# Performance work log

Hardware: AMD Instinct MI355X
Metric: run time of the kernel (lower is better)

## Reference

```python
import jax, jax.numpy as jnp
import numpy as np

B, S, HID = 1, 4096, 2048
NH, D = 16, 128
RATIO, TOPK, WIN = 4, 8, 128
ROPE_DIM = D // 2  # partial RoPE on first half of head_dim
EPS = 1e-6
NEG = -1e30


def rmsnorm(x, w):
    return x * jax.lax.rsqrt(jnp.mean(x * x, axis=-1, keepdims=True) + EPS) * w


def apply_rope(x, pos):
    # x: [..., L, D_head]; pos: [L] integer positions
    half = ROPE_DIM // 2
    inv = 1.0 / (10000.0 ** (jnp.arange(half, dtype=x.dtype) * (2.0 / ROPE_DIM)))
    ang = pos.astype(x.dtype)[:, None] * inv[None, :]  # [L, half]
    cos, sin = jnp.cos(ang), jnp.sin(ang)
    x1, x2, rest = x[..., :half], x[..., half:ROPE_DIM], x[..., ROPE_DIM:]
    return jnp.concatenate([x1 * cos - x2 * sin, x1 * sin + x2 * cos, rest], axis=-1)


def setup_inputs() -> dict:
    key = jax.random.key(0)
    ks = jax.random.split(key, 16)
    n = jax.random.normal
    s = 0.02
    return {
        "hidden_states": n(ks[0], (B, S, HID), jnp.float32),
        "Wq": n(ks[1], (HID, NH * D)) * s, "bq": jnp.zeros((NH * D,)),
        "Wcmp": n(ks[2], (HID, 1)) * s, "bcmp": jnp.zeros((1,)),
        "Wk": n(ks[3], (HID, D)) * s, "bk": jnp.zeros((D,)),
        "Wv": n(ks[4], (HID, D)) * s, "bv": jnp.zeros((D,)),
        "Wlk": n(ks[5], (HID, NH * D)) * s, "blk": jnp.zeros((NH * D,)),
        "Wlv": n(ks[6], (HID, NH * D)) * s, "blv": jnp.zeros((NH * D,)),
        "qn_w": jnp.ones((D,)), "kn_w": jnp.ones((D,)),
        "Wo": n(ks[7], (NH * D, HID)) * s, "bo": jnp.zeros((HID,)),
    }


def reference(hidden_states, Wq, bq, Wcmp, bcmp, Wk, bk, Wv, bv, Wlk, blk, Wlv, blv, qn_w, kn_w, Wo, bo):
    Bq, Sq, _ = hidden_states.shape
    C = Sq // RATIO
    scale = 1.0 / jnp.sqrt(jnp.float32(D))
    pos = jnp.arange(Sq)

    q = (hidden_states @ Wq + bq).reshape(Bq, Sq, NH, D).transpose(0, 2, 1, 3)  # [B,H,S,D]
    q = apply_rope(rmsnorm(q, qn_w), pos)

    # learned KV compression: softmax-weighted pooling within each block of size RATIO
    w_log = (hidden_states @ Wcmp + bcmp).reshape(Bq, C, RATIO)
    w_cmp = jax.nn.softmax(w_log, axis=-1)
    entries = jnp.einsum('bcr,bcrh->bch', w_cmp, hidden_states.reshape(Bq, C, RATIO, HID))
    block_ends = jnp.arange(1, C + 1) * RATIO - 1  # [C] last position of each block

    ck = apply_rope(rmsnorm(entries @ Wk + bk, kn_w), block_ends)  # [B,C,D] shared kv head
    cv = entries @ Wv + bv  # [B,C,D]

    # top-k block-sparse attention over compressed entries (causal on block_ends)
    sc = jnp.einsum('bhsd,bcd->bhsc', q, ck) * scale  # [B,H,S,C]
    causal = block_ends[None, None, None, :] <= pos[None, None, :, None]
    sc = jnp.where(causal, sc, NEG)
    tv, ti = jax.lax.top_k(sc, TOPK)  # [B,H,S,K]
    sel = (tv > NEG / 2).astype(sc.dtype)
    m = jnp.max(tv, axis=-1, keepdims=True)
    e = jnp.exp(tv - m) * sel
    pw = e / jnp.maximum(e.sum(axis=-1, keepdims=True), 1e-9)
    v_g = cv[jnp.arange(Bq)[:, None, None, None], ti]  # [B,H,S,K,D] irregular gather
    ctx_sparse = jnp.einsum('bhsk,bhskd->bhsd', pw, v_g)

    lk = apply_rope(rmsnorm((hidden_states @ Wlk + blk).reshape(Bq, Sq, NH, D).transpose(0, 2, 1, 3), kn_w), pos)
    lv = (hidden_states @ Wlv + blv).reshape(Bq, Sq, NH, D).transpose(0, 2, 1, 3)
    nc = Sq // WIN
    qc = q.reshape(Bq, NH, nc, WIN, D)

    def windowize(x):
        prev = jnp.pad(x, ((0, 0), (0, 0), (WIN, 0), (0, 0)))[:, :, :-WIN].reshape(Bq, NH, nc, WIN, D)
        cur = x.reshape(Bq, NH, nc, WIN, D)
        return jnp.concatenate([prev, cur], axis=3)  # [B,H,nc,2W,D]

    kw, vw = windowize(lk), windowize(lv)
    i = jnp.arange(WIN)[:, None]
    j = jnp.arange(2 * WIN)[None, :]
    rel = i + WIN - j  # qpos - kpos within the chunk pair
    band = (rel >= 0) & (rel <= WIN)
    kpos_ok = (jnp.arange(nc)[:, None, None] * WIN - WIN + j[None]) >= 0  # zero-pad chunk invalid
    mask = band[None] & kpos_ok  # [nc,W,2W]
    sl = jnp.einsum('bhcqd,bhckd->bhcqk', qc, kw) * scale
    sl = jnp.where(mask[None, None], sl, NEG)
    pl = jax.nn.softmax(sl, axis=-1)
    ctx_local = jnp.einsum('bhcqk,bhckd->bhcqd', pl, vw).reshape(Bq, NH, Sq, D)

    merged = (ctx_sparse + ctx_local) * 0.5  # mean over the two branches
    out = merged.transpose(0, 2, 1, 3).reshape(Bq, Sq, NH * D) @ Wo + bo
    return out
```

## Files before the change

### kernel.cpp

```cpp
#include <hip/hip_runtime.h>
#include <hip/hip_bf16.h>
#include <hip/hip_fp16.h>
#include <stdint.h>

typedef __hip_bfloat16 bf16;
using bf16x8 = __attribute__((ext_vector_type(8))) short;
using half8  = __attribute__((ext_vector_type(8))) _Float16;
using f32x4  = __attribute__((ext_vector_type(4))) float;

#define S_LEN   4096
#define HID_    2048
#define NH_     16
#define D_      128
#define C_      1024
#define SCALE_  0.08838834764831845f
#define DESC_   (1.0 / 1048576.0)

__device__ __forceinline__ void storeC(float* p, float v) { *p = v; }
__device__ __forceinline__ void storeC(bf16* p, float v)  { *p = __float2bfloat16(v); }
__device__ __forceinline__ void split2(float x, _Float16& h, _Float16& l) {
  h = (_Float16)x; l = (_Float16)(x - (float)h);
}
__device__ __forceinline__ short bf2s(bf16 b) { short s; __builtin_memcpy(&s, &b, 2); return s; }

#define GLDS(src, dst) __builtin_amdgcn_global_load_lds( \
    (const __attribute__((address_space(1))) void*)(src), \
    (__attribute__((address_space(3))) void*)(dst), 16, 0, 0)


__device__ __forceinline__ void cvt_bias_body(int bxx, const float* __restrict__ src, bf16* __restrict__ dst,
                                              const float* bq, const float* blk, const float* blv,
                                              const float* bk, const float* bv, const float* bo,
                                              float* bQ, float* bLKLV, float* bKV, float* bO) {
  int i = (bxx * 256 + threadIdx.x) * 4;
  float4 v = *(const float4*)(src + i);
  bf16 o[4] = {__float2bfloat16(v.x), __float2bfloat16(v.y),
               __float2bfloat16(v.z), __float2bfloat16(v.w)};
  *(uint2*)(dst + i) = *(uint2*)o;
  int ib = bxx * 256 + threadIdx.x;
  if (ib < 8448) {
    if (ib < 2048)      bQ[ib] = bq[ib];
    else if (ib < 6144) { int j = ib - 2048; bLKLV[j] = (j < 2048) ? blk[j] : blv[j - 2048]; }
    else if (ib < 6400) { int j = ib - 6144; bKV[j] = (j < 128) ? bk[j] : bv[j - 128]; }
    else                bO[ib - 6400] = bo[ib - 6400];
  }
}

__device__ __forceinline__ void transpose3_body(int bxx, int byy, int bzz, char* smem,
                                                const float* __restrict__ Wlk, const float* __restrict__ Wlv,
                                                const float* __restrict__ Wo,
                                                bf16* __restrict__ bt_lklv, bf16* __restrict__ WoT) {
  float (*tile)[65] = (float(*)[65])smem;
  const float* src = (bzz == 0) ? Wlk : (bzz == 1) ? Wlv : Wo;
  bf16* dst = (bzz == 0) ? bt_lklv
            : (bzz == 1) ? (bt_lklv + (size_t)2048 * HID_) : WoT;
  const int c0 = bxx * 64, r0 = byy * 64;
  const int t = threadIdx.x, cc = t & 63, rb = t >> 6;
#pragma unroll
  for (int i = 0; i < 16; ++i) {
    int r = rb + i * 4;
    tile[r][cc] = src[(size_t)(r0 + r) * HID_ + c0 + cc];
  }
  __syncthreads();
#pragma unroll
  for (int i = 0; i < 16; ++i) {
    int r = rb + i * 4;
    dst[(size_t)(c0 + r) * HID_ + r0 + cc] = __float2bfloat16(tile[cc][r]);
  }
}

__device__ __forceinline__ void trans_kv_body(int bxx, int byy, int bzz, char* smem,
                                              const float* __restrict__ Wk, const float* __restrict__ Wv,
                                              float* __restrict__ WkvTs) {
  float (*tile)[65] = (float(*)[65])smem;
  const float* src = bzz ? Wv : Wk;
  float* dst = WkvTs + (bzz ? (size_t)128 * HID_ : 0);
  const int c0 = bxx * 64, r0 = byy * 64;
  const int t = threadIdx.x, cc = t & 63, rb = t >> 6;
#pragma unroll
  for (int i = 0; i < 16; ++i) {
    int r = rb + i * 4;
    tile[r][cc] = src[(size_t)(r0 + r) * 128 + c0 + cc];
  }
  __syncthreads();
#pragma unroll
  for (int i = 0; i < 16; ++i) {
    int r = rb + i * 4;
    dst[(size_t)(c0 + r) * HID_ + r0 + cc] = tile[cc][r] * 1024.0f;
  }
}

__device__ __forceinline__ void wlog_body(int bxx, const float* __restrict__ hidden,
                                          const float* __restrict__ wcmp, const float* __restrict__ bcmp,
                                          float* __restrict__ wlog) {
  int s = bxx * 4 + (threadIdx.x >> 6);
  int lane = threadIdx.x & 63;
  const float* hp = hidden + (size_t)s * HID_;
  double acc = 0.0;
  for (int i = lane; i < HID_; i += 64)
    acc += (double)hp[i] * (double)wcmp[i];
#pragma unroll
  for (int m = 32; m; m >>= 1) acc += __shfl_xor(acc, m, 64);
  if (lane == 0) wlog[s] = (float)(acc + (double)bcmp[0]);
}

__device__ __forceinline__ void split_q_body(int bxx, const float* __restrict__ src,
                                             _Float16* __restrict__ oh, _Float16* __restrict__ ol) {
  int i = (bxx * 256 + threadIdx.x) * 4;
  float4 v = *(const float4*)(src + i);
  float xs[4] = {v.x, v.y, v.z, v.w};
  _Float16 hh[4], ll[4];
#pragma unroll
  for (int e = 0; e < 4; ++e) split2(xs[e] * 1024.0f, hh[e], ll[e]);
  *(uint2*)(oh + i) = *(uint2*)hh;
  *(uint2*)(ol + i) = *(uint2*)ll;
}

__device__ __forceinline__ void trans_split_wq_body(int bxx, int byy, char* smem,
                                                    const float* __restrict__ src,
                                                    _Float16* __restrict__ oh, _Float16* __restrict__ ol) {
  float (*tile)[65] = (float(*)[65])smem;
  const int c0 = bxx * 64, r0 = byy * 64;
  const int t = threadIdx.x, cc = t & 63, rb = t >> 6;
#pragma unroll
  for (int i = 0; i < 16; ++i) {
    int r = rb + i * 4;
    tile[r][cc] = src[(size_t)(r0 + r) * HID_ + c0 + cc];
  }
  __syncthreads();
#pragma unroll
  for (int i = 0; i < 16; ++i) {
    int r = rb + i * 4;
    float x = tile[cc][r] * 1024.0f;
    _Float16 h, l; split2(x, h, l);
    size_t off = (size_t)(c0 + r) * HID_ + r0 + cc;
    oh[off] = h; ol[off] = l;
  }
}

__device__ __forceinline__ void entries_body(int bxx, const float* __restrict__ hidden,
                                             const float* __restrict__ wsm, float* __restrict__ entriesF) {
  int idx = bxx * 256 + threadIdx.x;
  int c = idx >> 11, hcol = idx & 2047;
  double e = 0.0;
#pragma unroll
  for (int r = 0; r < 4; ++r)
    e += (double)wsm[4 * c + r] * (double)hidden[(size_t)(4 * c + r) * HID_ + hcol];
  entriesF[idx] = (float)e;
}

template <typename OutT>
__device__ __forceinline__ void gemm_bt_body(int bxp, int byp, bf16* As, bf16* Bs,
                                             const bf16* __restrict__ A, const bf16* __restrict__ BT,
                                             const float* __restrict__ bias, OutT* __restrict__ Cmat,
                                             int M, int N, int K, int lda) {
  const int t = threadIdx.x;
  const int wave = t >> 6, lane = t & 63;
  const int wr = wave >> 1, wc = wave & 1;
  const int quad = lane >> 4, l15 = lane & 15;
  const int bx = bxp * 128, by = byp * 128;
  const int srow = t >> 2, scol = (t & 3) * 8;
  f32x4 acc[4][4] = {};
  const bf16* a0 = A + (size_t)(by + srow) * lda + scol;
  const bf16* a1 = A + (size_t)(by + 64 + srow) * lda + scol;
  const bf16* b0 = BT + (size_t)(bx + srow) * K + scol;
  const bf16* b1 = BT + (size_t)(bx + 64 + srow) * K + scol;
  for (int k0 = 0; k0 < K; k0 += 32) {
    GLDS(a0 + k0, As + t * 8);
    GLDS(a1 + k0, As + 2048 + t * 8);
    GLDS(b0 + k0, Bs + t * 8);
    GLDS(b1 + k0, Bs + 2048 + t * 8);
    __syncthreads();
    bf16x8 aF[4], bF[4];
#pragma unroll
    for (int i = 0; i < 4; ++i)
      aF[i] = *(const bf16x8*)(As + (wr * 64 + i * 16 + l15) * 32 + quad * 8);
#pragma unroll
    for (int j = 0; j < 4; ++j)
      bF[j] = *(const bf16x8*)(Bs + (wc * 64 + j * 16 + l15) * 32 + quad * 8);
#pragma unroll
    for (int i = 0; i < 4; ++i)
#pragma unroll
      for (int j = 0; j < 4; ++j)
        acc[i][j] = __builtin_amdgcn_mfma_f32_16x16x32_bf16(aF[i], bF[j], acc[i][j], 0, 0, 0);
    __syncthreads();
  }
#pragma unroll
  for (int i = 0; i < 4; ++i)
#pragma unroll
    for (int j = 0; j < 4; ++j)
#pragma unroll
      for (int r = 0; r < 4; ++r) {
        int row = by + wr * 64 + i * 16 + quad * 4 + r;
        int col = bx + wc * 64 + j * 16 + l15;
        storeC(&Cmat[(size_t)row * N + col], acc[i][j][r] + bias[col]);
      }
}

__device__ __forceinline__ void gemm_hl4_body(int bxp, int byp, _Float16* Ahs, _Float16* Als,
                                              _Float16* Bhs, _Float16* Bls,
                                              const _Float16* __restrict__ Ah, const _Float16* __restrict__ Al,
                                              const _Float16* __restrict__ Bh, const _Float16* __restrict__ Bl,
                                              const float* __restrict__ bias, float* __restrict__ Cmat,
                                              int M, int N, int K, int lda) {
  const int t = threadIdx.x;
  const int wave = t >> 6, lane = t & 63;
  const int wr = wave >> 1, wc = wave & 1;
  const int quad = lane >> 4, l15 = lane & 15;
  const int bx = bxp * 128, by = byp * 128;
  const int srow = t >> 2, scol = (t & 3) * 8;
  double acc[4][4][4] = {};
  const _Float16* a0h = Ah + (size_t)(by + srow) * lda + scol;
  const _Float16* a1h = Ah + (size_t)(by + 64 + srow) * lda + scol;
  const _Float16* a0l = Al + (size_t)(by + srow) * lda + scol;
  const _Float16* a1l = Al + (size_t)(by + 64 + srow) * lda + scol;
  const _Float16* b0h = Bh + (size_t)(bx + srow) * K + scol;
  const _Float16* b1h = Bh + (size_t)(bx + 64 + srow) * K + scol;
  const _Float16* b0l = Bl + (size_t)(bx + srow) * K + scol;
  const _Float16* b1l = Bl + (size_t)(bx + 64 + srow) * K + scol;
  for (int k0 = 0; k0 < K; k0 += 32) {
    GLDS(a0h + k0, Ahs + t * 8);
    GLDS(a1h + k0, Ahs + 2048 + t * 8);
    GLDS(a0l + k0, Als + t * 8);
    GLDS(a1l + k0, Als + 2048 + t * 8);
    GLDS(b0h + k0, Bhs + t * 8);
    GLDS(b1h + k0, Bhs + 2048 + t * 8);
    GLDS(b0l + k0, Bls + t * 8);
    GLDS(b1l + k0, Bls + 2048 + t * 8);
    __syncthreads();
    half8 aFh[4], aFl[4], bFh[4], bFl[4];
#pragma unroll
    for (int i = 0; i < 4; ++i) {
      int ro = (wr * 64 + i * 16 + l15) * 32 + quad * 8;
      aFh[i] = *(const half8*)(Ahs + ro);
      aFl[i] = *(const half8*)(Als + ro);
    }
#pragma unroll
    for (int j = 0; j < 4; ++j) {
      int ro = (wc * 64 + j * 16 + l15) * 32 + quad * 8;
      bFh[j] = *(const half8*)(Bhs + ro);
      bFl[j] = *(const half8*)(Bls + ro);
    }
#pragma unroll
    for (int i = 0; i < 4; ++i)
#pragma unroll
      for (int j = 0; j < 4; ++j) {
        f32x4 tt = {0.f, 0.f, 0.f, 0.f};
        tt = __builtin_amdgcn_mfma_f32_16x16x32_f16(aFl[i], bFl[j], tt, 0, 0, 0);
        tt = __builtin_amdgcn_mfma_f32_16x16x32_f16(aFl[i], bFh[j], tt, 0, 0, 0);
        tt = __builtin_amdgcn_mfma_f32_16x16x32_f16(aFh[i], bFl[j], tt, 0, 0, 0);
        tt = __builtin_amdgcn_mfma_f32_16x16x32_f16(aFh[i], bFh[j], tt, 0, 0, 0);
#pragma unroll
        for (int r = 0; r < 4; ++r) acc[i][j][r] += (double)tt[r];
      }
    __syncthreads();
  }
#pragma unroll
  for (int i = 0; i < 4; ++i)
#pragma unroll
    for (int j = 0; j < 4; ++j)
#pragma unroll
      for (int r = 0; r < 4; ++r) {
        int row = by + wr * 64 + i * 16 + quad * 4 + r;
        int col = bx + wc * 64 + j * 16 + l15;
        Cmat[(size_t)row * N + col] = (float)(acc[i][j][r] * DESC_ + (double)bias[col]);
      }
}

__device__ __forceinline__ void gemm_prec4_body(int bxp, int byp, _Float16* Ah, _Float16* Al,
                                                _Float16* Bh, _Float16* Bl,
                                                const float* __restrict__ A, const float* __restrict__ BT,
                                                const float* __restrict__ bias, float* __restrict__ Cmat,
                                                int M, int N, int K, int lda) {
  const int t = threadIdx.x;
  const int wave = t >> 6, lane = t & 63;
  const int wr = wave >> 1, wc = wave & 1;
  const int quad = lane >> 4, l15 = lane & 15;
  const int bx = bxp * 128, by = byp * 128;
  double acc[4][4][4] = {};
  for (int k0 = 0; k0 < K; k0 += 32) {
#pragma unroll
    for (int it = 0; it < 4; ++it) {
      int sl = t + it * 256;
      int isB = sl >> 9, s2 = sl & 511, r = s2 >> 2, g = s2 & 3;
      const float* src = isB ? (BT + (size_t)(bx + r) * K + k0 + g * 8)
                             : (A  + (size_t)(by + r) * lda + k0 + g * 8);
      float4 u = ((const float4*)src)[0];
      float4 v = ((const float4*)src)[1];
      float xs[8] = {u.x, u.y, u.z, u.w, v.x, v.y, v.z, v.w};
      half8 hh, ll;
#pragma unroll
      for (int e = 0; e < 8; ++e) {
        float x = isB ? xs[e] : xs[e] * 1024.0f;
        _Float16 h, l; split2(x, h, l);
        hh[e] = h; ll[e] = l;
      }
      _Float16* dh = (isB ? Bh : Ah) + r * 32 + g * 8;
      _Float16* dl = (isB ? Bl : Al) + r * 32 + g * 8;
      *(half8*)dh = hh;
      *(half8*)dl = ll;
    }
    __syncthreads();
    half8 aFh[4], aFl[4], bFh[4], bFl[4];
#pragma unroll
    for (int i = 0; i < 4; ++i) {
      int ro = (wr * 64 + i * 16 + l15) * 32 + quad * 8;
      aFh[i] = *(const half8*)(Ah + ro);
      aFl[i] = *(const half8*)(Al + ro);
    }
#pragma unroll
    for (int j = 0; j < 4; ++j) {
      int ro = (wc * 64 + j * 16 + l15) * 32 + quad * 8;
      bFh[j] = *(const half8*)(Bh + ro);
      bFl[j] = *(const half8*)(Bl + ro);
    }
#pragma unroll
    for (int i = 0; i < 4; ++i)
#pragma unroll
      for (int j = 0; j < 4; ++j) {
        f32x4 tt = {0.f, 0.f, 0.f, 0.f};
        tt = __builtin_amdgcn_mfma_f32_16x16x32_f16(aFl[i], bFl[j], tt, 0, 0, 0);
        tt = __builtin_amdgcn_mfma_f32_16x16x32_f16(aFl[i], bFh[j], tt, 0, 0, 0);
        tt = __builtin_amdgcn_mfma_f32_16x16x32_f16(aFh[i], bFl[j], tt, 0, 0, 0);
        tt = __builtin_amdgcn_mfma_f32_16x16x32_f16(aFh[i], bFh[j], tt, 0, 0, 0);
#pragma unroll
        for (int r = 0; r < 4; ++r) acc[i][j][r] += (double)tt[r];
      }
    __syncthreads();
  }
#pragma unroll
  for (int i = 0; i < 4; ++i)
#pragma unroll
    for (int j = 0; j < 4; ++j)
#pragma unroll
      for (int r = 0; r < 4; ++r) {
        int row = by + wr * 64 + i * 16 + quad * 4 + r;
        int col = bx + wc * 64 + j * 16 + l15;
        Cmat[(size_t)row * N + col] = (float)(acc[i][j][r] * DESC_ + (double)bias[col]);
      }
}

__device__ __forceinline__ void normrope_q_body(int s, double* csd, double* snd,
                                                float* __restrict__ base, const float* __restrict__ w,
                                                _Float16* __restrict__ qh, _Float16* __restrict__ ql) {
  const int t = threadIdx.x, wv = t >> 6, lane = t & 63;
  if (t < 32) {
    float invf = 1.0f / (float)pow(10000.0, (double)t * (1.0 / 32.0));
    float angf = (float)s * invf;
    double ang = (double)angf;
    csd[t] = cos(ang);
    snd[t] = sin(ang);
  }
  __syncthreads();
  const int fi = lane & 31;
  float* ps = base + (size_t)s * HID_;
  for (int h = wv; h < 16; h += 4) {
    float* p = ps + h * 128;
    double x0 = (double)p[lane];
    double x1 = (double)p[lane + 64];
    double ss = x0 * x0 + x1 * x1;
#pragma unroll
    for (int m = 32; m; m >>= 1) ss += __shfl_xor(ss, m, 64);
    double rstd = 1.0 / sqrt(ss * (1.0 / 128.0) + 1e-6);
    double n0 = x0 * rstd * (double)w[lane];
    double n1 = x1 * rstd * (double)w[lane + 64];
    double other = __shfl_xor(n0, 32, 64);
    double cs = csd[fi], sn = snd[fi];
    double r0 = (lane < 32) ? (n0 * cs - other * sn) : (other * sn + n0 * cs);
    float f0 = (float)r0, f1 = (float)n1;
    p[lane] = f0;
    p[lane + 64] = f1;
    _Float16 h0, l0, h1, l1;
    split2(f0 * 1024.0f, h0, l0);
    split2(f1 * 1024.0f, h1, l1);
    size_t off = (size_t)s * HID_ + h * 128;
    qh[off + lane] = h0;       ql[off + lane] = l0;
    qh[off + 64 + lane] = h1;  ql[off + 64 + lane] = l1;
  }
}

__device__ __forceinline__ void normrope_ck_body(int bxx, float* __restrict__ base, const float* __restrict__ w,
                                                 _Float16* __restrict__ ckh, _Float16* __restrict__ ckl) {
  int row = bxx * 4 + (threadIdx.x >> 6);
  int lane = threadIdx.x & 63;
  float* p = base + (size_t)row * 256;
  double x0 = (double)p[lane];
  double x1 = (double)p[lane + 64];
  double ss = x0 * x0 + x1 * x1;
#pragma unroll
  for (int m = 32; m; m >>= 1) ss += __shfl_xor(ss, m, 64);
  double rstd = 1.0 / sqrt(ss * (1.0 / 128.0) + 1e-6);
  double n0 = x0 * rstd * (double)w[lane];
  double n1 = x1 * rstd * (double)w[lane + 64];
  double other = __shfl_xor(n0, 32, 64);
  int fi = lane & 31;
  float invf = 1.0f / (float)pow(10000.0, (double)fi * (1.0 / 32.0));
  float angf = (float)(row * 4 + 3) * invf;
  double ang = (double)angf;
  double cs = cos(ang), sn = sin(ang);
  double r0 = (lane < 32) ? (n0 * cs - other * sn) : (other * sn + n0 * cs);
  float f0 = (float)r0, f1 = (float)n1;
  p[lane] = f0;
  p[lane + 64] = f1;
  _Float16 h0, l0, h1, l1;
  split2(f0 * 1024.0f, h0, l0);
  split2(f1 * 1024.0f, h1, l1);
  ckh[row * 128 + lane] = h0;       ckl[row * 128 + lane] = l0;
  ckh[row * 128 + 64 + lane] = h1;  ckl[row * 128 + 64 + lane] = l1;
}

__device__ __forceinline__ void normrope_bfl_body(int s, float* csf, float* snf,
                                                  bf16* __restrict__ base, const float* __restrict__ w) {
  const int t = threadIdx.x, wv = t >> 6, lane = t & 63;
  if (t < 32) {
    float invf = 1.0f / (float)pow(10000.0, (double)t * (1.0 / 32.0));
    float ang = (float)s * invf;
    csf[t] = cosf(ang);
    snf[t] = sinf(ang);
  }
  __syncthreads();
  const int fi = lane & 31;
  bf16* ps = base + (size_t)s * 4096;
  for (int h = wv; h < 16; h += 4) {
    bf16* p = ps + h * 128;
    float x0 = __bfloat162float(p[lane]);
    float x1 = __bfloat162float(p[lane + 64]);
    float ss = x0 * x0 + x1 * x1;
#pragma unroll
    for (int m = 32; m; m >>= 1) ss += __shfl_xor(ss, m, 64);
    float rstd = rsqrtf(ss * 0.0078125f + 1e-6f);
    float n0 = x0 * rstd * w[lane];
    float n1 = x1 * rstd * w[lane + 64];
    float other = __shfl_xor(n0, 32, 64);
    float cs = csf[fi], sn = snf[fi];
    float r0 = (lane < 32) ? (n0 * cs - other * sn) : (other * sn + n0 * cs);
    p[lane] = __float2bfloat16(r0);
    p[lane + 64] = __float2bfloat16(n1);
  }
}


__global__ __launch_bounds__(256) void prep_fused(const float* hidden, bf16* hbf,
                                                  const float* Wlk, const float* Wlv, const float* Wo,
                                                  bf16* bt_lklv, bf16* WoT,
                                                  const float* Wk, const float* Wv, float* WkvTs,
                                                  const float* wcmp, const float* bcmp, float* wlog,
                                                  const float* bq, const float* blk, const float* blv,
                                                  const float* bk, const float* bv, const float* bo,
                                                  float* bQ, float* bLKLV, float* bKV, float* bO) {
  __shared__ __align__(16) char smem[16640];
  int b = blockIdx.x;
  if (b < 3072) {
    int z = b >> 10, rem = b & 1023;
    transpose3_body(rem & 31, rem >> 5, z, smem, Wlk, Wlv, Wo, bt_lklv, WoT);
  } else if (b < 3200) {
    int tt = b - 3072;
    trans_kv_body(tt & 1, (tt & 63) >> 1, tt >> 6, smem, Wk, Wv, WkvTs);
  } else if (b < 11392) {
    cvt_bias_body(b - 3200, hidden, hbf, bq, blk, blv, bk, bv, bo, bQ, bLKLV, bKV, bO);
  } else {
    wlog_body(b - 11392, hidden, wcmp, bcmp, wlog);
  }
}

__global__ void wsm_k(const float* __restrict__ wlog, float* __restrict__ wsm) {
  int c = blockIdx.x * 256 + threadIdx.x;
  if (c >= C_) return;
  double v[4], m = -1e300;
#pragma unroll
  for (int r = 0; r < 4; ++r) { v[r] = (double)wlog[4 * c + r]; if (v[r] > m) m = v[r]; }
  double sum = 0.0;
#pragma unroll
  for (int r = 0; r < 4; ++r) { v[r] = exp(v[r] - m); sum += v[r]; }
#pragma unroll
  for (int r = 0; r < 4; ++r) wsm[4 * c + r] = (float)(v[r] / sum);
}

__global__ __launch_bounds__(256) void lklv_entries_fused(const bf16* hbf, const bf16* bt_lklv,
                                                          const float* bLKLV, bf16* lklv,
                                                          const float* hidden, const float* wsm,
                                                          float* entriesF) {
  __shared__ __align__(16) bf16 AsBs[2][4096];
  int b = blockIdx.x;
  if (b < 1024) {
    gemm_bt_body<bf16>(b & 31, b >> 5, AsBs[0], AsBs[1], hbf, bt_lklv, bLKLV, lklv,
                       S_LEN, 4096, HID_, HID_);
  } else {
    entries_body(b - 1024, hidden, wsm, entriesF);
  }
}

__global__ __launch_bounds__(256) void splitq_fused(const float* hidden, _Float16* hidh, _Float16* hidl,
                                                    const float* Wq, _Float16* wqh, _Float16* wql) {
  __shared__ __align__(16) char smem[16640];
  int b = blockIdx.x;
  if (b < 1024) {
    trans_split_wq_body(b & 31, b >> 5, smem, Wq, wqh, wql);
  } else {
    split_q_body(b - 1024, hidden, hidh, hidl);
  }
}

__global__ __launch_bounds__(256) void qgemm_fused(const _Float16* hidh, const _Float16* hidl,
                                                   const _Float16* wqh, const _Float16* wql,
                                                   const float* bQ, float* qf,
                                                   const float* entriesF, const float* WkvTs,
                                                   const float* bKV, float* ckvF) {
  __shared__ __align__(16) _Float16 SH4[4][4096];
  int b = blockIdx.x;
  if (b < 512) {
    gemm_hl4_body(b & 15, b >> 4, SH4[0], SH4[1], SH4[2], SH4[3],
                  hidh, hidl, wqh, wql, bQ, qf, S_LEN, HID_, HID_, HID_);
  } else {
    int tt = b - 512;
    gemm_prec4_body(tt & 1, tt >> 1, SH4[0], SH4[1], SH4[2], SH4[3],
                    entriesF, WkvTs, bKV, ckvF, C_, 256, HID_, HID_);
  }
}

__global__ __launch_bounds__(256) void normrope_fused(float* qf, const float* qn_w,
                                                      _Float16* qh, _Float16* ql,
                                                      float* ckvF, const float* kn_w,
                                                      _Float16* ckh, _Float16* ckl,
                                                      bf16* lklv) {
  __shared__ double csd[32], snd[32];
  __shared__ float csf[32], snf[32];
  int b = blockIdx.x;
  if (b < 256) {
    normrope_ck_body(b, ckvF, kn_w, ckh, ckl);
  } else if (b < 4352) {
    normrope_q_body(b - 256, csd, snd, qf, qn_w, qh, ql);
  } else {
    normrope_bfl_body(b - 4352, csf, snf, lklv, kn_w);
  }
}

__global__ __launch_bounds__(256) void trans_v_k(const bf16* __restrict__ lklv, bf16* __restrict__ VT) {
  __shared__ ushort tile[64][65];
  const int s0 = blockIdx.x * 64, c0 = blockIdx.y * 64;
  const int t = threadIdx.x, cc = t & 63, rb = t >> 6;
  const ushort* src = (const ushort*)lklv;
#pragma unroll
  for (int i = 0; i < 16; ++i) {
    int r = rb + i * 4;
    tile[r][cc] = src[(size_t)(s0 + r) * 4096 + 2048 + c0 + cc];
  }
  __syncthreads();
  ushort* dst = (ushort*)VT;
#pragma unroll
  for (int i = 0; i < 16; ++i) {
    int r = rb + i * 4;
    dst[(size_t)(c0 + r) * 4096 + s0 + cc] = tile[cc][r];
  }
}

template <typename OutT>
__global__ __launch_bounds__(256) void gemm_bt(const bf16* __restrict__ A, const bf16* __restrict__ BT,
                                               const float* __restrict__ bias, OutT* __restrict__ Cmat,
                                               int M, int N, int K, int lda) {
  __shared__ __align__(16) bf16 AsBs[2][4096];
  gemm_bt_body<OutT>(blockIdx.x, blockIdx.y, AsBs[0], AsBs[1], A, BT, bias, Cmat, M, N, K, lda);
}

__global__ __launch_bounds__(1024, 8) void sparse_v9(const _Float16* __restrict__ qh, const _Float16* __restrict__ ql,
                                                     const _Float16* __restrict__ ckh, const _Float16* __restrict__ ckl,
                                                     const float* __restrict__ ckvF, bf16* __restrict__ sp) {
  __shared__ float sc[16 * 1024];
  const int by = blockIdx.y;
  const int s0 = blockIdx.x * 8;
  const int t = threadIdx.x, w = t >> 6, lane = t & 63;
  const int quad = lane >> 4, l15 = lane & 15;
  const int nvmax  = (s0 >> 2) + 2;
  const int ntiles = (nvmax + 15) >> 4;
  const double esc = (double)SCALE_ * DESC_;

  if (w < ntiles) {
    const int sA = s0 + (l15 & 7);
    const int hA = 2 * by + (l15 >> 3);
    half8 aFh[4], aFl[4];
    {
      const _Float16* qbh = qh + (size_t)sA * HID_ + hA * 128 + quad * 8;
      const _Float16* qbl = ql + (size_t)sA * HID_ + hA * 128 + quad * 8;
#pragma unroll
      for (int kk = 0; kk < 4; ++kk) {
        aFh[kk] = *(const half8*)(qbh + kk * 32);
        aFl[kk] = *(const half8*)(qbl + kk * 32);
      }
    }
    for (int ct = w; ct < ntiles; ct += 16) {
      const int c0 = ct * 16;
      const _Float16* kbh = ckh + (size_t)(c0 + l15) * 128 + quad * 8;
      const _Float16* kbl = ckl + (size_t)(c0 + l15) * 128 + quad * 8;
      double a64[4] = {0.0, 0.0, 0.0, 0.0};
#pragma unroll
      for (int kk = 0; kk < 4; ++kk) {
        half8 bh = *(const half8*)(kbh + kk * 32);
        half8 bl = *(const half8*)(kbl + kk * 32);
        f32x4 tt = {0.f, 0.f, 0.f, 0.f};
        tt = __builtin_amdgcn_mfma_f32_16x16x32_f16(aFl[kk], bl, tt, 0, 0, 0);
        tt = __builtin_amdgcn_mfma_f32_16x16x32_f16(aFl[kk], bh, tt, 0, 0, 0);
        tt = __builtin_amdgcn_mfma_f32_16x16x32_f16(aFh[kk], bl, tt, 0, 0, 0);
        tt = __builtin_amdgcn_mfma_f32_16x16x32_f16(aFh[kk], bh, tt, 0, 0, 0);
#pragma unroll
        for (int r = 0; r < 4; ++r) a64[r] += (double)tt[r];
      }
#pragma unroll
      for (int r = 0; r < 4; ++r)
        sc[(quad * 4 + r) * 1024 + c0 + l15] = (float)(a64[r] * esc);
    }
  }
  __syncthreads();
  if (w >= 4) return;

  const int q = w * 4 + quad;
  const int p2 = q >> 3, wq = q & 7;
  const int s = s0 + wq;
  const int nv = (s >= 3) ? (((s - 3) >> 2) + 1) : 0;
  const float* srow = sc + q * 1024;
  const int jmaxB = (nvmax + 63) >> 6;

  float tv0 = -1e38f, tv1 = -1e38f, tv2 = -1e38f, tv3 = -1e38f;
  int   ti0 = 0x40000000, ti1 = 0x40000000, ti2 = 0x40000000, ti3 = 0x40000000;
  for (int j = 0; j < jmaxB; ++j) {
    int cb = j * 64 + l15 * 4;
    float4 vv = *(const float4*)(srow + cb);
    float xs[4] = {vv.x, vv.y, vv.z, vv.w};
#pragma unroll
    for (int e = 0; e < 4; ++e) {
      int c = cb + e;
      float v = (c < nv) ? xs[e] : -1e38f;
      if (v > tv3) {
        if (v > tv0)      { tv3=tv2;ti3=ti2; tv2=tv1;ti2=ti1; tv1=tv0;ti1=ti0; tv0=v;ti0=c; }
        else if (v > tv1) { tv3=tv2;ti3=ti2; tv2=tv1;ti2=ti1; tv1=v;ti1=c; }
        else if (v > tv2) { tv3=tv2;ti3=ti2; tv2=v;ti2=c; }
        else              { tv3=v;ti3=c; }
      }
    }
  }

  unsigned long long deadm = 0ull;
  int ncons = 0;
  float bvs[8]; int bis[8];
#pragma unroll
  for (int it = 0; it < 8; ++it) {
    float bv = tv0; int bi = ti0;
#pragma unroll
    for (int mm = 1; mm <= 8; mm <<= 1) {
      float ov = __shfl_xor(bv, mm, 64);
      int   oi = __shfl_xor(bi, mm, 64);
      if (ov > bv || (ov == bv && oi < bi)) { bv = ov; bi = oi; }
    }
    bvs[it] = bv; bis[it] = bi;
    if (bv > -1e29f && (((bi >> 2) & 15) == l15)) {
      deadm |= 1ull << (((bi >> 6) << 2) | (bi & 3));
      tv0=tv1;ti0=ti1; tv1=tv2;ti1=ti2; tv2=tv3;ti2=ti3;
      tv3=-1e38f; ti3=0x40000000;
      if (++ncons == 4) {
        ncons = 0;
        tv0=tv1=tv2=tv3=-1e38f;
        ti0=ti1=ti2=ti3=0x40000000;
        for (int j = 0; j < jmaxB; ++j) {
          int cb = j * 64 + l15 * 4;
          float4 vv = *(const float4*)(srow + cb);
          float xs[4] = {vv.x, vv.y, vv.z, vv.w};
#pragma unroll
          for (int e = 0; e < 4; ++e) {
            int c = cb + e;
            int li = ((c >> 6) << 2) | (c & 3);
            float v = (c < nv && !((deadm >> li) & 1ull)) ? xs[e] : -1e38f;
            if (v > tv3) {
              if (v > tv0)      { tv3=tv2;ti3=ti2; tv2=tv1;ti2=ti1; tv1=tv0;ti1=ti0; tv0=v;ti0=c; }
              else if (v > tv1) { tv3=tv2;ti3=ti2; tv2=tv1;ti2=ti1; tv1=v;ti1=c; }
              else if (v > tv2) { tv3=tv2;ti3=ti2; tv2=v;ti2=c; }
              else              { tv3=v;ti3=c; }
            }
          }
        }
      }
    }
  }

  const float m0 = bvs[0];
  float a0=0.f,a1=0.f,a2=0.f,a3=0.f,a4=0.f,a5=0.f,a6=0.f,a7=0.f;
  float esum = 0.f;
#pragma unroll
  for (int it = 0; it < 8; ++it) {
    if (bvs[it] > -1e29f) {
      float wgt = expf(bvs[it] - m0);
      esum += wgt;
      const float* cvp = ckvF + (size_t)bis[it] * 256 + 128 + l15 * 8;
      float4 u = *(const float4*)cvp;
      float4 v = *(const float4*)(cvp + 4);
      a0 += wgt*u.x; a1 += wgt*u.y; a2 += wgt*u.z; a3 += wgt*u.w;
      a4 += wgt*v.x; a5 += wgt*v.y; a6 += wgt*v.z; a7 += wgt*v.w;
    }
  }
  float inv = 1.0f / fmaxf(esum, 1e-9f);
  bf16* op = sp + (size_t)s * 2048 + (2 * by + p2) * 128 + l15 * 8;
  bf16 ob[8] = {__float2bfloat16(a0*inv), __float2bfloat16(a1*inv),
                __float2bfloat16(a2*inv), __float2bfloat16(a3*inv),
                __float2bfloat16(a4*inv), __float2bfloat16(a5*inv),
                __float2bfloat16(a6*inv), __float2bfloat16(a7*inv)};
  *(uint4*)op = *(uint4*)ob;
}

__global__ __launch_bounds__(128) void local_mfma(const float* __restrict__ qf,
                                                  const bf16* __restrict__ lklv,
                                                  const bf16* __restrict__ VT,
                                                  const bf16* __restrict__ sp,
                                                  bf16* __restrict__ merged) {
  constexpr int PADP = 168;
  __shared__ bf16 PhS[2][16 * PADP];
  __shared__ bf16 PlS[2][16 * PADP];
  const int h = blockIdx.y;
  const int t = threadIdx.x, w = t >> 6, lane = t & 63;
  const int quad = lane >> 4, l15 = lane & 15;
  const int sw = blockIdx.x * 32 + w * 16;
  const int kbase = sw - 128;
  const int ridx = quad * 4;

  bf16x8 qH[4], qL[4];
  {
    const float* qp = qf + (size_t)(sw + l15) * HID_ + h * 128 + quad * 8;
#pragma unroll
    for (int kk = 0; kk < 4; ++kk) {
      float4 u = *(const float4*)(qp + kk * 32);
      float4 v = *(const float4*)(qp + kk * 32 + 4);
      float xs[8] = {u.x, u.y, u.z, u.w, v.x, v.y, v.z, v.w};
      bf16x8 hh, ll;
#pragma unroll
      for (int e = 0; e < 8; ++e) {
        bf16 bh = __float2bfloat16(xs[e]);
        float fh = __bfloat162float(bh);
        bf16 bl = __float2bfloat16(xs[e] - fh);
        hh[e] = bf2s(bh); ll[e] = bf2s(bl);
      }
      qH[kk] = hh; qL[kk] = ll;
    }
  }

  float sc[9][4];
#pragma unroll
  for (int ct = 0; ct < 9; ++ct) {
    int key0 = kbase + ct * 16 + l15;
    const bf16* kp = lklv + (size_t)(key0 < 0 ? 0 : key0) * 4096 + h * 128 + quad * 8;
    f32x4 acc = {0.f, 0.f, 0.f, 0.f};
#pragma unroll
    for (int kk = 0; kk < 4; ++kk) {
      bf16x8 kb = *(const bf16x8*)(kp + kk * 32);
      acc = __builtin_amdgcn_mfma_f32_16x16x32_bf16(qL[kk], kb, acc, 0, 0, 0);
      acc = __builtin_amdgcn_mfma_f32_16x16x32_bf16(qH[kk], kb, acc, 0, 0, 0);
    }
#pragma unroll
    for (int r = 0; r < 4; ++r) sc[ct][r] = acc[r] * SCALE_;
  }

  float mrow[4] = {-1e30f, -1e30f, -1e30f, -1e30f};
#pragma unroll
  for (int ct = 0; ct < 9; ++ct) {
    int cidx = ct * 16 + l15;
#pragma unroll
    for (int r = 0; r < 4; ++r) {
      bool valid = (cidx >= ridx + r) && (cidx <= ridx + r + 128) && (kbase + cidx >= 0);
      float v = valid ? sc[ct][r] : -1e30f;
      sc[ct][r] = v;
      mrow[r] = fmaxf(mrow[r], v);
    }
  }
#pragma unroll
  for (int mm = 1; mm <= 8; mm <<= 1)
#pragma unroll
    for (int r = 0; r < 4; ++r) mrow[r] = fmaxf(mrow[r], __shfl_xor(mrow[r], mm, 64));

  bf16* phb = &PhS[w][0];
  bf16* plb = &PlS[w][0];
  for (int z = lane; z < 256; z += 64) {
    int zr = z >> 4, zc = z & 15;
    phb[zr * PADP + 144 + zc] = __float2bfloat16(0.f);
    plb[zr * PADP + 144 + zc] = __float2bfloat16(0.f);
  }
  float lsum[4] = {0.f, 0.f, 0.f, 0.f};
#pragma unroll
  for (int ct = 0; ct < 9; ++ct) {
    int cidx = ct * 16 + l15;
#pragma unroll
    for (int r = 0; r < 4; ++r) {
      float e = (sc[ct][r] > -1e29f) ? expf(sc[ct][r] - mrow[r]) : 0.f;
      lsum[r] += e;
      bf16 bh = __float2bfloat16(e);
      float fh = __bfloat162float(bh);
      bf16 bl = __float2bfloat16(e - fh);
      phb[(ridx + r) * PADP + cidx] = bh;
      plb[(ridx + r) * PADP + cidx] = bl;
    }
  }
#pragma unroll
  for (int mm = 1; mm <= 8; mm <<= 1)
#pragma unroll
    for (int r = 0; r < 4; ++r) lsum[r] += __shfl_xor(lsum[r], mm, 64);
  float inv[4];
#pragma unroll
  for (int r = 0; r < 4; ++r) inv[r] = 1.0f / lsum[r];

  bf16x8 pH[5], pL[5];
#pragma unroll
  for (int kk = 0; kk < 5; ++kk) {
    pH[kk] = *(const bf16x8*)(phb + l15 * PADP + kk * 32 + quad * 8);
    pL[kk] = *(const bf16x8*)(plb + l15 * PADP + kk * 32 + quad * 8);
  }

#pragma unroll
  for (int dt = 0; dt < 8; ++dt) {
    const bf16* vrow = VT + (size_t)(h * 128 + dt * 16 + l15) * 4096;
    f32x4 acc = {0.f, 0.f, 0.f, 0.f};
#pragma unroll
    for (int kk = 0; kk < 5; ++kk) {
      int ko = kbase + kk * 32 + quad * 8;
      ko = ko < 0 ? 0 : (ko > 4088 ? 4088 : ko);
      bf16x8 vb = *(const bf16x8*)(vrow + ko);
      acc = __builtin_amdgcn_mfma_f32_16x16x32_bf16(pL[kk], vb, acc, 0, 0, 0);
      acc = __builtin_amdgcn_mfma_f32_16x16x32_bf16(pH[kk], vb, acc, 0, 0, 0);
    }
#pragma unroll
    for (int r = 0; r < 4; ++r) {
      int srow = sw + ridx + r;
      size_t off = (size_t)srow * 2048 + h * 128 + dt * 16 + l15;
      float spv = __bfloat162float(sp[off]);
      merged[off] = __float2bfloat16((acc[r] * inv[r] + spv) * 0.5f);
    }
  }
}

extern "C" void kernel_launch(void* const* d_in, const int* in_sizes, int n_in,
                              void* d_out, int out_size, void* d_ws, size_t ws_size,
                              hipStream_t stream) {
  (void)in_sizes; (void)n_in; (void)out_size; (void)ws_size;
  const float* hidden = (const float*)d_in[0];
  const float* Wq   = (const float*)d_in[1];
  const float* bq   = (const float*)d_in[2];
  const float* Wcmp = (const float*)d_in[3];
  const float* bcmp = (const float*)d_in[4];
  const float* Wk   = (const float*)d_in[5];
  const float* bk   = (const float*)d_in[6];
  const float* Wv   = (const float*)d_in[7];
  const float* bv   = (const float*)d_in[8];
  const float* Wlk  = (const float*)d_in[9];
  const float* blk  = (const float*)d_in[10];
  const float* Wlv  = (const float*)d_in[11];
  const float* blv  = (const float*)d_in[12];
  const float* qn_w = (const float*)d_in[13];
  const float* kn_w = (const float*)d_in[14];
  const float* Wo   = (const float*)d_in[15];
  const float* bo   = (const float*)d_in[16];
  float* out = (float*)d_out;

  char* ws = (char*)d_ws;
  float*    qf       = (float*)   (ws);
  bf16*     lklv     = (bf16*)    (ws + 33554432);
  _Float16* qh       = (_Float16*)(ws + 67108864);
  bf16*     VT       = (bf16*)    (ws + 67108864);
  bf16*     hbf      = (bf16*)    (ws + 83886080);
  _Float16* hidh     = (_Float16*)(ws + 83886080);
  bf16*     merged   = (bf16*)    (ws + 83886080);
  bf16*     bt_lklv  = (bf16*)    (ws + 100663296);
  _Float16* hidl     = (_Float16*)(ws + 100663296);
  bf16*     sp       = (bf16*)    (ws + 100663296);
  float*    WkvTs    = (float*)   (ws + 117440512);
  bf16*     WoT      = (bf16*)    (ws + 119537664);
  float*    entriesF = (float*)   (ws + 127926272);
  float*    ckvF     = (float*)   (ws + 136314880);
  _Float16* ckh      = (_Float16*)(ws + 137363456);
  _Float16* ckl      = (_Float16*)(ws + 137625600);
  float*    wlog     = (float*)   (ws + 137887744);
  float*    wsm      = (float*)   (ws + 137904128);
  float*    bQ       = (float*)   (ws + 137920512);
  float*    bLKLV    = (float*)   (ws + 137928704);
  float*    bKV      = (float*)   (ws + 137945088);
  float*    bO       = (float*)   (ws + 137946112);
  _Float16* wqh      = (_Float16*)(ws + 137954304);
  _Float16* wql      = (_Float16*)(ws + 146342912);
  _Float16* ql       = (_Float16*)(ws + 137954304);

  prep_fused<<<dim3(12416), dim3(256), 0, stream>>>(hidden, hbf, Wlk, Wlv, Wo, bt_lklv, WoT,
                                                    Wk, Wv, WkvTs, Wcmp, bcmp, wlog,
                                                    bq, blk, blv, bk, bv, bo, bQ, bLKLV, bKV, bO);
  wsm_k<<<dim3(4), dim3(256), 0, stream>>>(wlog, wsm);
  lklv_entries_fused<<<dim3(9216), dim3(256), 0, stream>>>(hbf, bt_lklv, bLKLV, lklv,
                                                           hidden, wsm, entriesF);
  splitq_fused<<<dim3(9216), dim3(256), 0, stream>>>(hidden, hidh, hidl, Wq, wqh, wql);
  qgemm_fused<<<dim3(528), dim3(256), 0, stream>>>(hidh, hidl, wqh, wql, bQ, qf,
                                                   entriesF, WkvTs, bKV, ckvF);
  normrope_fused<<<dim3(8448), dim3(256), 0, stream>>>(qf, qn_w, qh, ql, ckvF, kn_w, ckh, ckl, lklv);
  sparse_v9<<<dim3(512, 8), dim3(1024), 0, stream>>>(qh, ql, ckh, ckl, ckvF, sp);
  trans_v_k<<<dim3(64, 32), dim3(256), 0, stream>>>(lklv, VT);
  local_mfma<<<dim3(128, 16), dim3(128), 0, stream>>>(qf, lklv, VT, sp, merged);
  gemm_bt<float><<<dim3(16, 32), dim3(256), 0, stream>>>(merged, WoT, bO, out, S_LEN, HID_, HID_, HID_);
}
```

Baseline: 997.7 us.

## Halve Q-GEMM tile width, swizzle LDS fragments, schedule slow blocks first

The split-half fp16 Q projection GEMM now uses 128x64 tiles instead of 128x128, which doubles the block count so more blocks are in flight on the GPU, and halves the double-precision accumulator registers per thread. Global-to-LDS loads use an XOR swizzle on the 8-element column groups, and fragment reads undo it, to reduce LDS bank conflicts. The long-K ck/cv precision GEMM blocks are moved to the front of the grid so they start early. The cost is less operand reuse per tile, since each A tile is now loaded twice as often.

After: 887.7 us. -11.0%, faster.

```diff
diff --git a/kernel.cpp b/kernel.cpp
--- a/kernel.cpp
+++ b/kernel.cpp
@@ -197,54 +197,55 @@
       }
 }
 
-__device__ __forceinline__ void gemm_hl4_body(int bxp, int byp, _Float16* Ahs, _Float16* Als,
-                                              _Float16* Bhs, _Float16* Bls,
-                                              const _Float16* __restrict__ Ah, const _Float16* __restrict__ Al,
-                                              const _Float16* __restrict__ Bh, const _Float16* __restrict__ Bl,
-                                              const float* __restrict__ bias, float* __restrict__ Cmat,
-                                              int M, int N, int K, int lda) {
+__device__ __forceinline__ void gemm_hl4b_body(int bxp, int byp, _Float16* Ahs, _Float16* Als,
+                                               _Float16* Bhs, _Float16* Bls,
+                                               const _Float16* __restrict__ Ah, const _Float16* __restrict__ Al,
+                                               const _Float16* __restrict__ Bh, const _Float16* __restrict__ Bl,
+                                               const float* __restrict__ bias, float* __restrict__ Cmat,
+                                               int N, int K, int lda) {
   const int t = threadIdx.x;
   const int wave = t >> 6, lane = t & 63;
   const int wr = wave >> 1, wc = wave & 1;
   const int quad = lane >> 4, l15 = lane & 15;
-  const int bx = bxp * 128, by = byp * 128;
-  const int srow = t >> 2, scol = (t & 3) * 8;
-  double acc[4][4][4] = {};
-  const _Float16* a0h = Ah + (size_t)(by + srow) * lda + scol;
-  const _Float16* a1h = Ah + (size_t)(by + 64 + srow) * lda + scol;
-  const _Float16* a0l = Al + (size_t)(by + srow) * lda + scol;
-  const _Float16* a1l = Al + (size_t)(by + 64 + srow) * lda + scol;
-  const _Float16* b0h = Bh + (size_t)(bx + srow) * K + scol;
-  const _Float16* b1h = Bh + (size_t)(bx + 64 + srow) * K + scol;
-  const _Float16* b0l = Bl + (size_t)(bx + srow) * K + scol;
-  const _Float16* b1l = Bl + (size_t)(bx + 64 + srow) * K + scol;
+  const int bx = bxp * 64, by = byp * 128;
+  const int rA0 = t >> 2;
+  const int rA1 = rA0 + 64;
+  const int g   = t & 3;
+  const int gsA0 = g ^ ((rA0 >> 1) & 3);
+  const int gsA1 = g ^ ((rA1 >> 1) & 3);
+  const int swz  = (l15 >> 1) & 3;
+  double acc[4][2][4] = {};
+  const _Float16* a0h = Ah + (size_t)(by + rA0) * lda + gsA0 * 8;
+  const _Float16* a1h = Ah + (size_t)(by + rA1) * lda + gsA1 * 8;
+  const _Float16* a0l = Al + (size_t)(by + rA0) * lda + gsA0 * 8;
+  const _Float16* a1l = Al + (size_t)(by + rA1) * lda + gsA1 * 8;
+  const _Float16* b0h = Bh + (size_t)(bx + rA0) * K + gsA0 * 8;
+  const _Float16* b0l = Bl + (size_t)(bx + rA0) * K + gsA0 * 8;
   for (int k0 = 0; k0 < K; k0 += 32) {
     GLDS(a0h + k0, Ahs + t * 8);
     GLDS(a1h + k0, Ahs + 2048 + t * 8);
     GLDS(a0l + k0, Als + t * 8);
     GLDS(a1l + k0, Als + 2048 + t * 8);
     GLDS(b0h + k0, Bhs + t * 8);
-    GLDS(b1h + k0, Bhs + 2048 + t * 8);
     GLDS(b0l + k0, Bls + t * 8);
-    GLDS(b1l + k0, Bls + 2048 + t * 8);
     __syncthreads();
-    half8 aFh[4], aFl[4], bFh[4], bFl[4];
+    half8 aFh[4], aFl[4], bFh[2], bFl[2];
 #pragma unroll
     for (int i = 0; i < 4; ++i) {
-      int ro = (wr * 64 + i * 16 + l15) * 32 + quad * 8;
+      int ro = (wr * 64 + i * 16 + l15) * 32 + (quad ^ swz) * 8;
       aFh[i] = *(const half8*)(Ahs + ro);
       aFl[i] = *(const half8*)(Als + ro);
     }
 #pragma unroll
-    for (int j = 0; j < 4; ++j) {
-      int ro = (wc * 64 + j * 16 + l15) * 32 + quad * 8;
+    for (int j = 0; j < 2; ++j) {
+      int ro = (wc * 32 + j * 16 + l15) * 32 + (quad ^ swz) * 8;
       bFh[j] = *(const half8*)(Bhs + ro);
       bFl[j] = *(const half8*)(Bls + ro);
     }
 #pragma unroll
     for (int i = 0; i < 4; ++i)
 #pragma unroll
-      for (int j = 0; j < 4; ++j) {
+      for (int j = 0; j < 2; ++j) {
         f32x4 tt = {0.f, 0.f, 0.f, 0.f};
         tt = __builtin_amdgcn_mfma_f32_16x16x32_f16(aFl[i], bFl[j], tt, 0, 0, 0);
         tt = __builtin_amdgcn_mfma_f32_16x16x32_f16(aFl[i], bFh[j], tt, 0, 0, 0);
@@ -258,11 +259,11 @@
 #pragma unroll
   for (int i = 0; i < 4; ++i)
 #pragma unroll
-    for (int j = 0; j < 4; ++j)
+    for (int j = 0; j < 2; ++j)
 #pragma unroll
       for (int r = 0; r < 4; ++r) {
         int row = by + wr * 64 + i * 16 + quad * 4 + r;
-        int col = bx + wc * 64 + j * 16 + l15;
+        int col = bx + wc * 32 + j * 16 + l15;
         Cmat[(size_t)row * N + col] = (float)(acc[i][j][r] * DESC_ + (double)bias[col]);
       }
 }
@@ -508,13 +509,13 @@
                                                    const float* bKV, float* ckvF) {
   __shared__ __align__(16) _Float16 SH4[4][4096];
   int b = blockIdx.x;
-  if (b < 512) {
-    gemm_hl4_body(b & 15, b >> 4, SH4[0], SH4[1], SH4[2], SH4[3],
-                  hidh, hidl, wqh, wql, bQ, qf, S_LEN, HID_, HID_, HID_);
+  if (b < 16) {
+    gemm_prec4_body(b & 1, b >> 1, SH4[0], SH4[1], SH4[2], SH4[3],
+                    entriesF, WkvTs, bKV, ckvF, C_, 256, HID_, HID_);
   } else {
-    int tt = b - 512;
-    gemm_prec4_body(tt & 1, tt >> 1, SH4[0], SH4[1], SH4[2], SH4[3],
-                    entriesF, WkvTs, bKV, ckvF, C_, 256, HID_, HID_);
+    int bb = b - 16;
+    gemm_hl4b_body(bb & 31, bb >> 5, SH4[0], SH4[1], SH4[2], SH4[3],
+                   hidh, hidl, wqh, wql, bQ, qf, HID_, HID_, HID_);
   }
 }
 
@@ -888,8 +889,8 @@
   lklv_entries_fused<<<dim3(9216), dim3(256), 0, stream>>>(hbf, bt_lklv, bLKLV, lklv,
                                                            hidden, wsm, entriesF);
   splitq_fused<<<dim3(9216), dim3(256), 0, stream>>>(hidden, hidh, hidl, Wq, wqh, wql);
-  qgemm_fused<<<dim3(528), dim3(256), 0, stream>>>(hidh, hidl, wqh, wql, bQ, qf,
-                                                   entriesF, WkvTs, bKV, ckvF);
+  qgemm_fused<<<dim3(1040), dim3(256), 0, stream>>>(hidh, hidl, wqh, wql, bQ, qf,
+                                                    entriesF, WkvTs, bKV, ckvF);
   normrope_fused<<<dim3(8448), dim3(256), 0, stream>>>(qf, qn_w, qh, ql, ckvF, kn_w, ckh, ckl, lklv);
   sparse_v9<<<dim3(512, 8), dim3(1024), 0, stream>>>(qh, ql, ckh, ckl, ckvF, sp);
   trans_v_k<<<dim3(64, 32), dim3(256), 0, stream>>>(lklv, VT);
```
